# Kernel optimization log

Hardware: AMD Instinct MI355X
Metric: run time of the kernel (lower is better)

Reference implementation:

```python
import jax, jax.numpy as jnp
import numpy as np

B, S, D, H = 2, 2048, 1024, 16
HD = D // H


def setup_inputs() -> dict:
    key = jax.random.key(0)
    ks = jax.random.split(key, 5)
    scale = 0.02
    x = jax.random.normal(ks[0], (B, S, D), dtype=jnp.float32)
    Wq = jax.random.normal(ks[1], (D, D), dtype=jnp.float32) * scale
    Wk = jax.random.normal(ks[2], (D, D), dtype=jnp.float32) * scale
    Wv = jax.random.normal(ks[3], (D, D), dtype=jnp.float32) * scale
    Wo = jax.random.normal(ks[4], (D, D), dtype=jnp.float32) * scale
    z = jnp.zeros((D,), dtype=jnp.float32)
    return {"x": x, "Wq": Wq, "bq": z, "Wk": Wk, "bk": z, "Wv": Wv, "bv": z, "Wo": Wo, "bo": z}


def reference(x, Wq, bq, Wk, bk, Wv, bv, Wo, bo):
    b, s, d = x.shape
    hd = d // H
    # QKV projections -> [b, H, s, hd]
    def heads(W, bias):
        return (x @ W.T + bias).reshape(b, s, H, hd).transpose(0, 2, 1, 3)
    q = heads(Wq, bq)
    k = heads(Wk, bk)
    v = heads(Wv, bv)
    scale = 1.0 / np.sqrt(hd).astype(np.float32)
    attn = scale * jnp.einsum('bhqd,bhkd->bhqk', q, k)  # [b,H,s,s]
    # causal mask (attn dropout p=0 is identity before masking)
    causal = jnp.tril(jnp.ones((s, s), dtype=bool))
    attn = jnp.where(causal[None, None], attn, -jnp.inf)
    attn = jax.nn.softmax(attn, axis=-1)
    ans = jnp.einsum('bhqk,bhkd->bhqd', attn, v)
    ans = ans.transpose(0, 2, 1, 3).reshape(b, s, d)
    return ans @ Wo.T + bo
```

## Files before the change

### kernel.cpp

```cpp
#include <hip/hip_runtime.h>

#define DEV __device__ __forceinline__

typedef __attribute__((ext_vector_type(8))) __bf16 bf16x8;
typedef __attribute__((ext_vector_type(4))) float f32x4;
typedef __attribute__((ext_vector_type(16))) float f32x16;
typedef __attribute__((ext_vector_type(4))) unsigned short u16x4;
typedef __attribute__((ext_vector_type(8))) unsigned short u16x8;
typedef __attribute__((ext_vector_type(2))) unsigned u32x2;

DEV unsigned short f2bf(float f) {
  unsigned u = __builtin_bit_cast(unsigned, f);
  u += 0x7FFFu + ((u >> 16) & 1u);
  return (unsigned short)(u >> 16);
}

DEV f32x4 mfma16(bf16x8 a, bf16x8 b, f32x4 c) {
  return __builtin_amdgcn_mfma_f32_16x16x32_bf16(a, b, c, 0, 0, 0);
}
DEV f32x16 mfma32(bf16x8 a, bf16x8 b, f32x16 c) {
  return __builtin_amdgcn_mfma_f32_32x32x16_bf16(a, b, c, 0, 0, 0);
}

DEV void gload16(const void* g, void* l) {
  __builtin_amdgcn_global_load_lds(
      (const __attribute__((address_space(1))) unsigned int*)g,
      (__attribute__((address_space(3))) unsigned int*)l, 16, 0, 0);
}

DEV void plswap(unsigned& x, unsigned& y) {
#if __has_builtin(__builtin_amdgcn_permlane32_swap)
  u32x2 r = __builtin_amdgcn_permlane32_swap(x, y, false, false);
  x = r[0];
  y = r[1];
#else
  unsigned sx = __shfl_xor(x, 32, 64), sy = __shfl_xor(y, 32, 64);
  int hi = (threadIdx.x & 63) >> 5;
  unsigned nx = hi ? sy : x;
  unsigned ny = hi ? y : sx;
  x = nx;
  y = ny;
#endif
}
DEV float xadd32(float v) {
  unsigned a = __builtin_bit_cast(unsigned, v), b = a;
  plswap(a, b);
  return __builtin_bit_cast(float, a) + __builtin_bit_cast(float, b);
}

__global__ __launch_bounds__(256) void k_cvt_all(
    const float* __restrict__ x,
    const float* __restrict__ Wq, const float* __restrict__ Wk,
    const float* __restrict__ Wv, const float* __restrict__ Wo,
    unsigned short* __restrict__ xb,
    unsigned short* __restrict__ Wqb, unsigned short* __restrict__ Wkb,
    unsigned short* __restrict__ Wvb, unsigned short* __restrict__ Wob) {
  int g = blockIdx.x * 256 + threadIdx.x;
  const float* src;
  unsigned short* dst;
  int loc;
  if (g < 524288) {
    src = x; dst = xb; loc = g;
  } else {
    int r = g - 524288;
    int w = r >> 17;
    loc = r & 131071;
    src = w == 0 ? Wq : w == 1 ? Wk : w == 2 ? Wv : Wo;
    dst = w == 0 ? Wqb : w == 1 ? Wkb : w == 2 ? Wvb : Wob;
  }
  int row = loc >> 7, k8 = loc & 127;
  const f32x4* s = (const f32x4*)(src + ((size_t)row << 10) + (k8 << 3));
  f32x4 a = s[0], b = s[1];
  u16x8 o;
  o[0] = f2bf(a[0]); o[1] = f2bf(a[1]); o[2] = f2bf(a[2]); o[3] = f2bf(a[3]);
  o[4] = f2bf(b[0]); o[5] = f2bf(b[1]); o[6] = f2bf(b[2]); o[7] = f2bf(b[3]);
  *(u16x8*)(dst + ((size_t)row << 10) + ((k8 << 3) ^ ((row & 7) << 3))) = o;
}

DEV void gemm_mainloop(const char* Ag, const char* Bg, char* lds,
                       int lane, int wid, f32x4 acc[4][4]) {
  int g4 = lane >> 4, r16 = lane & 15;
  int wm = wid >> 1, wn = wid & 1;
  int adA[2], adB[2];
#pragma unroll
  for (int ks = 0; ks < 2; ++ks) {
    int swz = ((ks * 4 + g4) ^ (lane & 7)) << 4;
    adA[ks] = (wm * 64 + r16) * 128 + swz;
    adB[ks] = 16384 + (wn * 64 + r16) * 128 + swz;
  }
  int o0 = wid * 4096 + lane * 16;
  int grow[4], ginr[4];
#pragma unroll
  for (int i = 0; i < 4; ++i) {
    grow[i] = (o0 + i * 1024) >> 7;
    ginr[i] = (o0 + i * 1024) & 127;
  }
  auto STAGE = [&](int KT, int BASE) {
#pragma unroll
    for (int i = 0; i < 4; ++i) {
      int oo = o0 + i * 1024;
      size_t gofs = (size_t)grow[i] * 2048 + (size_t)KT * 128 + ginr[i];
      gload16(Ag + gofs, lds + BASE + oo);
      gload16(Bg + gofs, lds + BASE + 16384 + oo);
    }
  };
  STAGE(0, 0);
  __syncthreads();
  for (int kt = 0; kt < 16; ++kt) {
    int cur = (kt & 1) << 15;
    if (kt + 1 < 16) STAGE(kt + 1, cur ^ 32768);
#pragma unroll
    for (int ks = 0; ks < 2; ++ks) {
      bf16x8 af[4], bfr[4];
#pragma unroll
      for (int i = 0; i < 4; ++i) {
        af[i]  = *(const bf16x8*)(lds + cur + adA[ks] + i * 2048);
        bfr[i] = *(const bf16x8*)(lds + cur + adB[ks] + i * 2048);
      }
#pragma unroll
      for (int mi = 0; mi < 4; ++mi)
#pragma unroll
        for (int ni = 0; ni < 4; ++ni)
          acc[mi][ni] = mfma16(af[mi], bfr[ni], acc[mi][ni]);
    }
    __syncthreads();
  }
}

__global__ __launch_bounds__(256) void k_gemm_qkv(
    const unsigned short* __restrict__ xb,
    const unsigned short* __restrict__ Wqb, const unsigned short* __restrict__ Wkb,
    const unsigned short* __restrict__ Wvb,
    const float* __restrict__ bq, const float* __restrict__ bk,
    const float* __restrict__ bv,
    unsigned short* __restrict__ Qb, unsigned short* __restrict__ Kb,
    unsigned short* __restrict__ Vt) {
  __shared__ char lds[65536];
  int tid = threadIdx.x, lane = tid & 63, wid = tid >> 6;
  int bm = blockIdx.x & 31, bn = blockIdx.x >> 5;
  int r0 = bm * 128;
  int colT = bn * 128;
  int which = colT >> 10;
  int ncol = colT & 1023;
  const unsigned short* Wb = which == 0 ? Wqb : which == 1 ? Wkb : Wvb;
  f32x4 acc[4][4] = {};
  gemm_mainloop((const char*)xb + (size_t)r0 * 2048,
                (const char*)Wb + (size_t)ncol * 2048, lds, lane, wid, acc);
  int g4 = lane >> 4, r16 = lane & 15, wm = wid >> 1, wn = wid & 1;
  const float* bias = which == 0 ? bq : which == 1 ? bk : bv;
  float oscale = which == 0 ? 0.18033688f : 1.0f;
  int ncolw = ncol + wn * 64;
#pragma unroll
  for (int ni = 0; ni < 4; ++ni) {
    int gcol = ncolw + ni * 16 + r16;
    float bvv = bias[gcol];
    int h = gcol >> 6, hd = gcol & 63;
#pragma unroll
    for (int mi = 0; mi < 4; ++mi) {
      int growb = r0 + wm * 64 + mi * 16 + g4 * 4;
      int bb = growb >> 11, s0 = growb & 2047;
      if (which == 2) {
        u16x4 pk;
#pragma unroll
        for (int jj = 0; jj < 4; ++jj) pk[jj] = f2bf(acc[mi][ni][jj] + bvv);
        *(u16x4*)(Vt + ((size_t)(bb * 16 + h) * 64 + hd) * 2048 + s0) = pk;
      } else {
        unsigned short* dst = which == 0 ? Qb : Kb;
        size_t base = ((size_t)(bb * 16 + h) * 2048 + s0) * 64 + hd;
#pragma unroll
        for (int jj = 0; jj < 4; ++jj)
          dst[base + (size_t)jj * 64] = f2bf((acc[mi][ni][jj] + bvv) * oscale);
      }
    }
  }
}

__global__ __launch_bounds__(128) void k_attn(
    const unsigned short* __restrict__ Q, const unsigned short* __restrict__ K,
    const unsigned short* __restrict__ Vt, unsigned short* __restrict__ ansb,
    float* __restrict__ PO, float* __restrict__ PL) {
  __shared__ char lds[2 * 8192 + 256];
  int tid = threadIdx.x, lane = tid & 63, wid = tid >> 6;
  int l31 = lane & 31, hi = lane >> 5;
  int bid = blockIdx.x;
  int bh = (bid & 7) * 4 + ((bid >> 3) & 3);
  int sden = bid >> 5;
  int c, j, nseg;
  if (sden < 8)       { c = sden; j = 0; nseg = 1; }
  else if (sden < 24) { int u = sden - 8;  c = 8  + (u >> 1); j = u & 1; nseg = 2; }
  else if (sden < 48) { int u = sden - 24; int q3 = u / 3; c = 16 + q3; j = u - 3 * q3; nseg = 3; }
  else                { int u = sden - 48; c = 24 + (u >> 2); j = u & 3; nseg = 4; }
  int t0 = j * (c + 1) / nseg, t1 = (j + 1) * (c + 1) / nseg;
  bool direct = (nseg == 1);
  int pidx = (bh * 24 + (c - 8)) * 4 + j;
  int b = bh >> 4, h = bh & 15;
  int q0 = c * 64 + wid * 32;
  const unsigned short* Qh = Q + (size_t)bh * (2048 * 64);
  const char* Kg = (const char*)(K + (size_t)bh * (2048 * 64));
  const char* Vg = (const char*)(Vt + (size_t)bh * (64 * 2048));
  char* wb = lds + 16384 + wid * 128;

  int kof[4], ko[4];
#pragma unroll
  for (int i = 0; i < 4; ++i) {
    int o = tid * 16 + i * 2048;
    int row = o >> 7, cc = o & 127;
    kof[i] = o;
    ko[i] = row * 128 + (cc ^ ((row & 7) << 4));
  }

  bf16x8 qf[4];
#pragma unroll
  for (int ks = 0; ks < 4; ++ks)
    qf[ks] = *(const bf16x8*)(Qh + (size_t)(q0 + l31) * 64 + ks * 16 + hi * 8);

  f32x16 O0 = {}, O1 = {}, l16 = {};
  int swzl = (l31 & 7) << 4;
  int hioff = hi * 16;
  const char* Vr0 = Vg + (size_t)l31 * 4096;
  const char* Vr1 = Vg + (size_t)(32 + l31) * 4096;

  auto STAGEK = [&](int T, int BASE) {
    size_t kK = (size_t)T * 8192;
#pragma unroll
    for (int i = 0; i < 4; ++i)
      gload16(Kg + kK + ko[i], lds + BASE + kof[i]);
  };

  STAGEK(t0, 0);
  __syncthreads();
  for (int t = t0; t < t1; ++t) {
    int cur = ((t - t0) & 1) << 13;
    if (t + 1 < t1) STAGEK(t + 1, cur ^ 8192);
    const char* KL = lds + cur;
    const char* Vt0 = Vr0 + (size_t)t * 128;
    const char* Vt1 = Vr1 + (size_t)t * 128;
    f32x16 s0 = {}, s1 = {};
    __builtin_amdgcn_s_setprio(1);
#pragma unroll
    for (int ks = 0; ks < 4; ++ks) {
      bf16x8 kf0 = *(const bf16x8*)(KL + l31 * 128 + ((ks * 32 + hioff) ^ swzl));
      bf16x8 kf1 = *(const bf16x8*)(KL + (32 + l31) * 128 + ((ks * 32 + hioff) ^ swzl));
      s0 = mfma32(kf0, qf[ks], s0);
      s1 = mfma32(kf1, qf[ks], s1);
    }
    __builtin_amdgcn_s_setprio(0);
    if (t == c) {
      int lim2 = q0 + l31 - t * 64 - 4 * hi;
#pragma unroll
      for (int r = 0; r < 16; ++r) {
        int kc = (r & 3) + 8 * (r >> 2);
        if (kc > lim2) s0[r] = -1e30f;
        if (kc + 32 > lim2) s1[r] = -1e30f;
      }
    }
#pragma unroll
    for (int r = 0; r < 16; ++r) {
      s0[r] = __builtin_amdgcn_exp2f(s0[r]);
      s1[r] = __builtin_amdgcn_exp2f(s1[r]);
      l16[r] += s0[r] + s1[r];
    }
    __builtin_amdgcn_s_setprio(1);
#define PV_CHUNK(SV, E, C16) { \
    unsigned x0, x1, y0, y1; \
    asm("v_cvt_pk_bf16_f32 %0, %1, %2" : "=v"(x0) : "v"(SV[8*(E)+0]), "v"(SV[8*(E)+1])); \
    asm("v_cvt_pk_bf16_f32 %0, %1, %2" : "=v"(x1) : "v"(SV[8*(E)+2]), "v"(SV[8*(E)+3])); \
    asm("v_cvt_pk_bf16_f32 %0, %1, %2" : "=v"(y0) : "v"(SV[8*(E)+4]), "v"(SV[8*(E)+5])); \
    asm("v_cvt_pk_bf16_f32 %0, %1, %2" : "=v"(y1) : "v"(SV[8*(E)+6]), "v"(SV[8*(E)+7])); \
    plswap(x0, y0); \
    plswap(x1, y1); \
    union { unsigned u[4]; bf16x8 v; } pf; \
    pf.u[0] = x0; \
    pf.u[1] = x1; \
    pf.u[2] = y0; \
    pf.u[3] = y1; \
    bf16x8 v0 = *(const bf16x8*)(Vt0 + (C16) * 32 + hi * 16); \
    bf16x8 v1 = *(const bf16x8*)(Vt1 + (C16) * 32 + hi * 16); \
    O0 = mfma32(pf.v, v0, O0); \
    O1 = mfma32(pf.v, v1, O1); }
    PV_CHUNK(s0, 0, 0)
    PV_CHUNK(s0, 1, 1)
    PV_CHUNK(s1, 0, 2)
    PV_CHUNK(s1, 1, 3)
#undef PV_CHUNK
    __builtin_amdgcn_s_setprio(0);
    __syncthreads();
  }
  float a[16];
#pragma unroll
  for (int r = 0; r < 16; ++r) a[r] = l16[r];
#pragma unroll
  for (int st2 = 8; st2 >= 1; st2 >>= 1)
#pragma unroll
    for (int i = 0; i < st2; ++i) a[i] += a[i + st2];
  float lf = xadd32(a[0]);
  if (direct) {
    float rl = 1.f / lf;
    if (lane < 32) *(float*)(wb + l31 * 4) = rl;
    asm volatile("s_waitcnt lgkmcnt(0)" ::: "memory");
    f32x4 rv0 = *(const f32x4*)(wb + hioff);
    f32x4 rv1 = *(const f32x4*)(wb + 32 + hioff);
    f32x4 rv2 = *(const f32x4*)(wb + 64 + hioff);
    f32x4 rv3 = *(const f32x4*)(wb + 96 + hioff);
#pragma unroll
    for (int r = 0; r < 16; ++r) {
      float sc = (r < 4 ? rv0 : r < 8 ? rv1 : r < 12 ? rv2 : rv3)[r & 3];
      int rowl = q0 + (r & 3) + 8 * (r >> 2) + 4 * hi;
      int rowg = (b << 11) + rowl;
      int cswz = (rowl & 7) << 3;
      int cg0 = (h << 6) + l31;
      int cg1 = (h << 6) + 32 + l31;
      ansb[(size_t)rowg * 1024 + (cg0 ^ cswz)] = f2bf(O0[r] * sc);
      ansb[(size_t)rowg * 1024 + (cg1 ^ cswz)] = f2bf(O1[r] * sc);
    }
  } else {
    float* po = PO + (size_t)pidx * 4096;
#pragma unroll
    for (int r = 0; r < 16; ++r) {
      int rowl = wid * 32 + (r & 3) + 8 * (r >> 2) + 4 * hi;
      po[rowl * 64 + l31] = O0[r];
      po[rowl * 64 + 32 + l31] = O1[r];
    }
    if (hi == 0) PL[pidx * 64 + wid * 32 + l31] = lf;
  }
}

__global__ __launch_bounds__(256) void k_attn_combine(
    const float* __restrict__ PO, const float* __restrict__ PL,
    unsigned short* __restrict__ ansb) {
  int bid = blockIdx.x;
  int bh = bid & 31, cc = 8 + (bid >> 5);
  int nseg = cc < 16 ? 2 : cc < 24 ? 3 : 4;
  int b = bh >> 4, h = bh & 15;
  int t = threadIdx.x;
  int r = t >> 2, c4 = (t & 3) << 4;
  int pbase = (bh * 24 + (cc - 8)) * 4;
  f32x4 s0 = {}, s1 = {}, s2 = {}, s3 = {};
  float lsum = 0.f;
  for (int j = 0; j < nseg; ++j) {
    const float* A = PO + (size_t)(pbase + j) * 4096 + r * 64 + c4;
    s0 += *(const f32x4*)(A + 0);
    s1 += *(const f32x4*)(A + 4);
    s2 += *(const f32x4*)(A + 8);
    s3 += *(const f32x4*)(A + 12);
    lsum += PL[(pbase + j) * 64 + r];
  }
  float rl = 1.f / lsum;
  u16x8 o0, o1;
#pragma unroll
  for (int j = 0; j < 4; ++j) {
    o0[j] = f2bf(s0[j] * rl);
    o0[4 + j] = f2bf(s1[j] * rl);
    o1[j] = f2bf(s2[j] * rl);
    o1[4 + j] = f2bf(s3[j] * rl);
  }
  int rowg = (b << 11) + cc * 64 + r;
  int colg = (h << 6) + c4;
  int cswz = (rowg & 7) << 3;
  *(u16x8*)(ansb + (size_t)rowg * 1024 + (colg ^ cswz)) = o0;
  *(u16x8*)(ansb + (size_t)rowg * 1024 + ((colg + 8) ^ cswz)) = o1;
}

__global__ __launch_bounds__(256) void k_gemm_out(
    const unsigned short* __restrict__ ansb, const unsigned short* __restrict__ Wob,
    const float* __restrict__ bo, float* __restrict__ out) {
  __shared__ char lds[65536];
  int tid = threadIdx.x, lane = tid & 63, wid = tid >> 6;
  int bm = blockIdx.x & 31, bn = blockIdx.x >> 5;
  int r0 = bm * 128, c0 = bn * 128;
  f32x4 acc[4][4] = {};
  gemm_mainloop((const char*)ansb + (size_t)r0 * 2048,
                (const char*)Wob + (size_t)c0 * 2048, lds, lane, wid, acc);
  int g4 = lane >> 4, r16 = lane & 15, wm = wid >> 1, wn = wid & 1;
#pragma unroll
  for (int ni = 0; ni < 4; ++ni) {
    int gcol = c0 + wn * 64 + ni * 16 + r16;
    float bvv = bo[gcol];
#pragma unroll
    for (int mi = 0; mi < 4; ++mi) {
      int growb = r0 + wm * 64 + mi * 16 + g4 * 4;
#pragma unroll
      for (int jj = 0; jj < 4; ++jj)
        out[(size_t)(growb + jj) * 1024 + gcol] = acc[mi][ni][jj] + bvv;
    }
  }
}

extern "C" void kernel_launch(void* const* d_in, const int* in_sizes, int n_in,
                              void* d_out, int out_size, void* d_ws, size_t ws_size,
                              hipStream_t stream) {
  const float* x  = (const float*)d_in[0];
  const float* Wq = (const float*)d_in[1];
  const float* bq = (const float*)d_in[2];
  const float* Wk = (const float*)d_in[3];
  const float* bk = (const float*)d_in[4];
  const float* Wv = (const float*)d_in[5];
  const float* bv = (const float*)d_in[6];
  const float* Wo = (const float*)d_in[7];
  const float* bo = (const float*)d_in[8];
  char* ws = (char*)d_ws;
  unsigned short* xb   = (unsigned short*)(ws);
  unsigned short* ansb = (unsigned short*)(ws);
  unsigned short* Wqb  = (unsigned short*)(ws + (8u  << 20));
  unsigned short* Wkb  = (unsigned short*)(ws + (10u << 20));
  unsigned short* Wvb  = (unsigned short*)(ws + (12u << 20));
  unsigned short* Wob  = (unsigned short*)(ws + (14u << 20));
  unsigned short* Qb   = (unsigned short*)(ws + (16u << 20));
  unsigned short* Kb   = (unsigned short*)(ws + (24u << 20));
  unsigned short* Vt   = (unsigned short*)(ws + (32u << 20));
  float*          PO   = (float*)(ws + (40u << 20));
  float*          PL   = (float*)(ws + (88u << 20));

  k_cvt_all<<<4096, 256, 0, stream>>>(x, Wq, Wk, Wv, Wo, xb, Wqb, Wkb, Wvb, Wob);
  k_gemm_qkv<<<768, 256, 0, stream>>>(xb, Wqb, Wkb, Wvb, bq, bk, bv, Qb, Kb, Vt);
  k_attn<<<2560, 128, 0, stream>>>(Qb, Kb, Vt, ansb, PO, PL);
  k_attn_combine<<<768, 256, 0, stream>>>(PO, PL, ansb);
  k_gemm_out<<<256, 256, 0, stream>>>(ansb, Wob, bo, (float*)d_out);
}
```

Baseline: 125.2 us.

## Stage V tiles through LDS and use table-driven causal work partition

The attention kernel now loads both K and V tiles into swizzled LDS each iteration, instead of double-buffering K and reading V fragments straight from global memory. It waits on all loads and a barrier before compute, so the K prefetch overlap is gone. The block-to-segment mapping is replaced by a constant lookup table that splits the causal query chunks unevenly across blocks to balance work. The gain relies on coalesced V staging and better load balance outweighing the lost overlap.

```diff
diff --git a/kernel.cpp b/kernel.cpp
--- a/kernel.cpp
+++ b/kernel.cpp
@@ -179,19 +179,45 @@
     const unsigned short* __restrict__ Q, const unsigned short* __restrict__ K,
     const unsigned short* __restrict__ Vt, unsigned short* __restrict__ ansb,
     float* __restrict__ PO, float* __restrict__ PL) {
-  __shared__ char lds[2 * 8192 + 256];
+  __shared__ char lds[16384 + 256];
+#define SG(c, a, bb2, jj) \
+  ((unsigned)(c) | ((unsigned)(a) << 8) | ((unsigned)(bb2) << 16) | ((unsigned)(jj) << 24))
+  static const unsigned SEGT[80] = {
+    SG(31,0,8,0),  SG(31,8,16,1), SG(31,16,24,2), SG(31,24,32,3),
+    SG(30,7,15,1), SG(30,15,23,2), SG(30,23,31,3),
+    SG(29,7,15,1), SG(29,22,30,3), SG(28,21,29,3),
+    SG(23,0,8,0),  SG(23,8,16,1), SG(23,16,24,2),
+    SG(22,7,15,1), SG(22,15,23,2), SG(21,14,22,2),
+    SG(15,0,8,0),  SG(15,8,16,1), SG(14,7,15,1),  SG(7,0,8,0),
+    SG(30,0,7,0),  SG(29,0,7,0),  SG(29,15,22,2),
+    SG(28,0,7,0),  SG(28,7,14,1), SG(28,14,21,2),
+    SG(27,0,7,0),  SG(27,7,14,1), SG(27,14,21,2), SG(27,21,28,3),
+    SG(26,6,13,1), SG(26,13,20,2), SG(26,20,27,3),
+    SG(25,6,13,1), SG(25,19,26,3), SG(24,18,25,3),
+    SG(22,0,7,0),  SG(21,0,7,0),  SG(21,7,14,1),
+    SG(20,0,7,0),  SG(20,7,14,1), SG(20,14,21,2),
+    SG(19,6,13,1), SG(19,13,20,2), SG(18,12,19,2),
+    SG(14,0,7,0),  SG(13,0,7,0),  SG(13,7,14,1),
+    SG(12,6,13,1), SG(6,0,7,0),
+    SG(26,0,6,0),  SG(25,0,6,0),  SG(25,13,19,2),
+    SG(24,0,6,0),  SG(24,6,12,1), SG(24,12,18,2),
+    SG(19,0,6,0),  SG(18,0,6,0),  SG(18,6,12,1),
+    SG(17,0,6,0),  SG(17,6,12,1), SG(17,12,18,2),
+    SG(16,5,11,1), SG(16,11,17,2),
+    SG(12,0,6,0),  SG(11,0,6,0),  SG(11,6,12,1),
+    SG(10,5,11,1), SG(5,0,6,0),
+    SG(16,0,5,0), SG(10,0,5,0), SG(9,0,5,0), SG(9,5,10,1), SG(8,4,9,1),
+    SG(4,0,5,0),
+    SG(8,0,4,0), SG(3,0,4,0), SG(2,0,3,0), SG(1,0,2,0), SG(0,0,1,0)
+  };
+#undef SG
   int tid = threadIdx.x, lane = tid & 63, wid = tid >> 6;
   int l31 = lane & 31, hi = lane >> 5;
   int bid = blockIdx.x;
   int bh = (bid & 7) * 4 + ((bid >> 3) & 3);
-  int sden = bid >> 5;
-  int c, j, nseg;
-  if (sden < 8)       { c = sden; j = 0; nseg = 1; }
-  else if (sden < 24) { int u = sden - 8;  c = 8  + (u >> 1); j = u & 1; nseg = 2; }
-  else if (sden < 48) { int u = sden - 24; int q3 = u / 3; c = 16 + q3; j = u - 3 * q3; nseg = 3; }
-  else                { int u = sden - 48; c = 24 + (u >> 2); j = u & 3; nseg = 4; }
-  int t0 = j * (c + 1) / nseg, t1 = (j + 1) * (c + 1) / nseg;
-  bool direct = (nseg == 1);
+  unsigned se = SEGT[bid >> 5];
+  int c = se & 255, t0 = (se >> 8) & 255, t1 = (se >> 16) & 255, j = se >> 24;
+  bool direct = (c < 8);
   int pidx = (bh * 24 + (c - 8)) * 4 + j;
   int b = bh >> 4, h = bh & 15;
   int q0 = c * 64 + wid * 32;
@@ -200,13 +226,15 @@
   const char* Vg = (const char*)(Vt + (size_t)bh * (64 * 2048));
   char* wb = lds + 16384 + wid * 128;
 
-  int kof[4], ko[4];
+  int kof[4], ko[4], vo[4];
 #pragma unroll
   for (int i = 0; i < 4; ++i) {
     int o = tid * 16 + i * 2048;
     int row = o >> 7, cc = o & 127;
+    int sc = cc ^ ((row & 7) << 4);
     kof[i] = o;
-    ko[i] = row * 128 + (cc ^ ((row & 7) << 4));
+    ko[i] = row * 128 + sc;
+    vo[i] = row * 4096 + sc;
   }
 
   bf16x8 qf[4];
@@ -217,24 +245,20 @@
   f32x16 O0 = {}, O1 = {}, l16 = {};
   int swzl = (l31 & 7) << 4;
   int hioff = hi * 16;
-  const char* Vr0 = Vg + (size_t)l31 * 4096;
-  const char* Vr1 = Vg + (size_t)(32 + l31) * 4096;
-
-  auto STAGEK = [&](int T, int BASE) {
-    size_t kK = (size_t)T * 8192;
-#pragma unroll
-    for (int i = 0; i < 4; ++i)
-      gload16(Kg + kK + ko[i], lds + BASE + kof[i]);
-  };
-
-  STAGEK(t0, 0);
-  __syncthreads();
+
   for (int t = t0; t < t1; ++t) {
-    int cur = ((t - t0) & 1) << 13;
-    if (t + 1 < t1) STAGEK(t + 1, cur ^ 8192);
-    const char* KL = lds + cur;
-    const char* Vt0 = Vr0 + (size_t)t * 128;
-    const char* Vt1 = Vr1 + (size_t)t * 128;
+    size_t kK = (size_t)t * 8192;
+    size_t kV = (size_t)t * 128;
+#pragma unroll
+    for (int i = 0; i < 4; ++i) {
+      gload16(Kg + kK + ko[i], lds + kof[i]);
+      gload16(Vg + kV + vo[i], lds + 8192 + kof[i]);
+    }
+    asm volatile("s_waitcnt vmcnt(0)" ::: "memory");
+    __builtin_amdgcn_s_barrier();
+    __builtin_amdgcn_sched_barrier(0);
+    const char* KL = lds;
+    const char* VL = lds + 8192;
     f32x16 s0 = {}, s1 = {};
     __builtin_amdgcn_s_setprio(1);
 #pragma unroll
@@ -274,8 +298,8 @@
     pf.u[1] = x1; \
     pf.u[2] = y0; \
     pf.u[3] = y1; \
-    bf16x8 v0 = *(const bf16x8*)(Vt0 + (C16) * 32 + hi * 16); \
-    bf16x8 v1 = *(const bf16x8*)(Vt1 + (C16) * 32 + hi * 16); \
+    bf16x8 v0 = *(const bf16x8*)(VL + l31 * 128 + (((C16) * 32 + hioff) ^ swzl)); \
+    bf16x8 v1 = *(const bf16x8*)(VL + (32 + l31) * 128 + (((C16) * 32 + hioff) ^ swzl)); \
     O0 = mfma32(pf.v, v0, O0); \
     O1 = mfma32(pf.v, v1, O1); }
     PV_CHUNK(s0, 0, 0)
```

New measurement: 109.9 us. -12.2%, faster.

## Restructure attention into single-wave 32-row tiles with LDS-staged V and finer barriers

Applied to the files above, without the earlier changes.

The attention kernel now runs one wave per block on 32-query tiles with 32-key steps. It stages both K and V tiles into swizzled LDS via async loads instead of reading V directly from global memory, and drops the block-wide barrier. The split-K schedule is rebuilt for the new tile count, heaviest tiles first, and the combine kernel is adapted to match. The GEMM mainloop replaces __syncthreads with explicit vmcnt/lgkmcnt waits, raw barriers and setprio around the MFMAs, to overlap the next stage's loads better. The cost is a doubled grid and more partial outputs, and per-block MFMA work is smaller, which may reduce efficiency.

```diff
diff --git a/kernel.cpp b/kernel.cpp
--- a/kernel.cpp
+++ b/kernel.cpp
@@ -105,10 +105,16 @@
     }
   };
   STAGE(0, 0);
-  __syncthreads();
   for (int kt = 0; kt < 16; ++kt) {
     int cur = (kt & 1) << 15;
-    if (kt + 1 < 16) STAGE(kt + 1, cur ^ 32768);
+    if (kt + 1 < 16) {
+      STAGE(kt + 1, cur ^ 32768);
+      asm volatile("s_waitcnt vmcnt(8)" ::: "memory");
+    } else {
+      asm volatile("s_waitcnt vmcnt(0)" ::: "memory");
+    }
+    __builtin_amdgcn_s_barrier();
+    __builtin_amdgcn_sched_barrier(0);
 #pragma unroll
     for (int ks = 0; ks < 2; ++ks) {
       bf16x8 af[4], bfr[4];
@@ -117,13 +123,17 @@
         af[i]  = *(const bf16x8*)(lds + cur + adA[ks] + i * 2048);
         bfr[i] = *(const bf16x8*)(lds + cur + adB[ks] + i * 2048);
       }
+      __builtin_amdgcn_s_setprio(1);
 #pragma unroll
       for (int mi = 0; mi < 4; ++mi)
 #pragma unroll
         for (int ni = 0; ni < 4; ++ni)
           acc[mi][ni] = mfma16(af[mi], bfr[ni], acc[mi][ni]);
-    }
-    __syncthreads();
+      __builtin_amdgcn_s_setprio(0);
+    }
+    asm volatile("s_waitcnt lgkmcnt(0)" ::: "memory");
+    __builtin_amdgcn_sched_barrier(0);
+    __builtin_amdgcn_s_barrier();
   }
 }
 
@@ -175,38 +185,40 @@
   }
 }
 
-__global__ __launch_bounds__(128) void k_attn(
+__global__ __launch_bounds__(64) void k_attn(
     const unsigned short* __restrict__ Q, const unsigned short* __restrict__ K,
     const unsigned short* __restrict__ Vt, unsigned short* __restrict__ ansb,
     float* __restrict__ PO, float* __restrict__ PL) {
-  __shared__ char lds[2 * 8192 + 256];
-  int tid = threadIdx.x, lane = tid & 63, wid = tid >> 6;
+  __shared__ char lds[2 * 8192 + 128];
+  int lane = threadIdx.x & 63;
   int l31 = lane & 31, hi = lane >> 5;
   int bid = blockIdx.x;
   int bh = (bid & 7) * 4 + ((bid >> 3) & 3);
   int sden = bid >> 5;
-  int c, j, nseg;
-  if (sden < 8)       { c = sden; j = 0; nseg = 1; }
-  else if (sden < 24) { int u = sden - 8;  c = 8  + (u >> 1); j = u & 1; nseg = 2; }
-  else if (sden < 48) { int u = sden - 24; int q3 = u / 3; c = 16 + q3; j = u - 3 * q3; nseg = 3; }
-  else                { int u = sden - 48; c = 24 + (u >> 2); j = u & 3; nseg = 4; }
-  int t0 = j * (c + 1) / nseg, t1 = (j + 1) * (c + 1) / nseg;
+  int cp, j, nseg;
+  if (sden < 8)        { cp = 15 - sden;          j = 0;              nseg = 1; }
+  else if (sden < 72)  { int u = sden - 8;   cp = 63 - (u >> 2); j = u & 3;        nseg = 4; }
+  else if (sden < 120) { int u = sden - 72;  int q3 = u / 3; cp = 47 - q3; j = u - 3 * q3; nseg = 3; }
+  else if (sden < 152) { int u = sden - 120; cp = 31 - (u >> 1); j = u & 1;        nseg = 2; }
+  else                 { int u = sden - 152; cp = 7 - u;           j = 0;          nseg = 1; }
+  int t0 = j * (cp + 1) / nseg, t1 = (j + 1) * (cp + 1) / nseg;
   bool direct = (nseg == 1);
-  int pidx = (bh * 24 + (c - 8)) * 4 + j;
+  int pidx = (bh * 48 + (cp - 16)) * 4 + j;
   int b = bh >> 4, h = bh & 15;
-  int q0 = c * 64 + wid * 32;
+  int q0 = cp * 32;
   const unsigned short* Qh = Q + (size_t)bh * (2048 * 64);
   const char* Kg = (const char*)(K + (size_t)bh * (2048 * 64));
   const char* Vg = (const char*)(Vt + (size_t)bh * (64 * 2048));
-  char* wb = lds + 16384 + wid * 128;
-
-  int kof[4], ko[4];
+
+  int kof[4], ko[4], vo[4];
 #pragma unroll
   for (int i = 0; i < 4; ++i) {
-    int o = tid * 16 + i * 2048;
+    int o = lane * 16 + i * 1024;
     int row = o >> 7, cc = o & 127;
     kof[i] = o;
     ko[i] = row * 128 + (cc ^ ((row & 7) << 4));
+    int vr = o >> 6, vc = o & 63;
+    vo[i] = vr * 4096 + (vc ^ (((vr >> 1) & 3) << 4));
   }
 
   bf16x8 qf[4];
@@ -216,49 +228,52 @@
 
   f32x16 O0 = {}, O1 = {}, l16 = {};
   int swzl = (l31 & 7) << 4;
+  int vswz = ((l31 >> 1) & 3) << 4;
   int hioff = hi * 16;
-  const char* Vr0 = Vg + (size_t)l31 * 4096;
-  const char* Vr1 = Vg + (size_t)(32 + l31) * 4096;
-
-  auto STAGEK = [&](int T, int BASE) {
-    size_t kK = (size_t)T * 8192;
-#pragma unroll
-    for (int i = 0; i < 4; ++i)
+
+  auto STAGEA = [&](int T, int BASE) {
+    size_t kK = (size_t)T * 4096;
+    size_t kV = (size_t)T * 64;
+#pragma unroll
+    for (int i = 0; i < 4; ++i) {
       gload16(Kg + kK + ko[i], lds + BASE + kof[i]);
+      gload16(Vg + kV + vo[i], lds + BASE + 4096 + kof[i]);
+    }
   };
 
-  STAGEK(t0, 0);
-  __syncthreads();
+  STAGEA(t0, 0);
   for (int t = t0; t < t1; ++t) {
     int cur = ((t - t0) & 1) << 13;
-    if (t + 1 < t1) STAGEK(t + 1, cur ^ 8192);
+    if (t + 1 < t1) {
+      asm volatile("s_waitcnt lgkmcnt(0)" ::: "memory");
+      STAGEA(t + 1, cur ^ 8192);
+      asm volatile("s_waitcnt vmcnt(8)" ::: "memory");
+    } else {
+      asm volatile("s_waitcnt vmcnt(0)" ::: "memory");
+    }
+    __builtin_amdgcn_sched_barrier(0);
     const char* KL = lds + cur;
-    const char* Vt0 = Vr0 + (size_t)t * 128;
-    const char* Vt1 = Vr1 + (size_t)t * 128;
-    f32x16 s0 = {}, s1 = {};
+    const char* VL = KL + 4096;
+    f32x16 s0 = {};
     __builtin_amdgcn_s_setprio(1);
 #pragma unroll
     for (int ks = 0; ks < 4; ++ks) {
       bf16x8 kf0 = *(const bf16x8*)(KL + l31 * 128 + ((ks * 32 + hioff) ^ swzl));
-      bf16x8 kf1 = *(const bf16x8*)(KL + (32 + l31) * 128 + ((ks * 32 + hioff) ^ swzl));
       s0 = mfma32(kf0, qf[ks], s0);
-      s1 = mfma32(kf1, qf[ks], s1);
     }
     __builtin_amdgcn_s_setprio(0);
-    if (t == c) {
-      int lim2 = q0 + l31 - t * 64 - 4 * hi;
+    if (t == cp) {
+      int lim2 = l31 - 4 * hi;
 #pragma unroll
       for (int r = 0; r < 16; ++r) {
         int kc = (r & 3) + 8 * (r >> 2);
         if (kc > lim2) s0[r] = -1e30f;
-        if (kc + 32 > lim2) s1[r] = -1e30f;
       }
     }
 #pragma unroll
     for (int r = 0; r < 16; ++r) {
       s0[r] = __builtin_amdgcn_exp2f(s0[r]);
-      s1[r] = __builtin_amdgcn_exp2f(s1[r]);
-      l16[r] += s0[r] + s1[r];
+      l16[r] += s0[r];
     }
     __builtin_amdgcn_s_setprio(1);
 #define PV_CHUNK(SV, E, C16) { \
@@ -274,17 +289,14 @@
     pf.u[1] = x1; \
     pf.u[2] = y0; \
     pf.u[3] = y1; \
-    bf16x8 v0 = *(const bf16x8*)(Vt0 + (C16) * 32 + hi * 16); \
-    bf16x8 v1 = *(const bf16x8*)(Vt1 + (C16) * 32 + hi * 16); \
+    bf16x8 v0 = *(const bf16x8*)(VL + l31 * 64 + (((C16) * 32 + hioff) ^ vswz)); \
+    bf16x8 v1 = *(const bf16x8*)(VL + (32 + l31) * 64 + (((C16) * 32 + hioff) ^ vswz)); \
     O0 = mfma32(pf.v, v0, O0); \
     O1 = mfma32(pf.v, v1, O1); }
     PV_CHUNK(s0, 0, 0)
     PV_CHUNK(s0, 1, 1)
-    PV_CHUNK(s1, 0, 2)
-    PV_CHUNK(s1, 1, 3)
 #undef PV_CHUNK
     __builtin_amdgcn_s_setprio(0);
-    __syncthreads();
   }
   float a[16];
 #pragma unroll
@@ -295,6 +307,8 @@
     for (int i = 0; i < st2; ++i) a[i] += a[i + st2];
   float lf = xadd32(a[0]);
   if (direct) {
+    asm volatile("s_waitcnt lgkmcnt(0)" ::: "memory");
+    char* wb = lds;
     float rl = 1.f / lf;
     if (lane < 32) *(float*)(wb + l31 * 4) = rl;
     asm volatile("s_waitcnt lgkmcnt(0)" ::: "memory");
@@ -314,36 +328,36 @@
       ansb[(size_t)rowg * 1024 + (cg1 ^ cswz)] = f2bf(O1[r] * sc);
     }
   } else {
-    float* po = PO + (size_t)pidx * 4096;
+    float* po = PO + (size_t)pidx * 2048;
 #pragma unroll
     for (int r = 0; r < 16; ++r) {
-      int rowl = wid * 32 + (r & 3) + 8 * (r >> 2) + 4 * hi;
+      int rowl = (r & 3) + 8 * (r >> 2) + 4 * hi;
       po[rowl * 64 + l31] = O0[r];
       po[rowl * 64 + 32 + l31] = O1[r];
     }
-    if (hi == 0) PL[pidx * 64 + wid * 32 + l31] = lf;
-  }
-}
-
-__global__ __launch_bounds__(256) void k_attn_combine(
+    if (hi == 0) PL[pidx * 32 + l31] = lf;
+  }
+}
+
+__global__ __launch_bounds__(128) void k_attn_combine(
     const float* __restrict__ PO, const float* __restrict__ PL,
     unsigned short* __restrict__ ansb) {
   int bid = blockIdx.x;
-  int bh = bid & 31, cc = 8 + (bid >> 5);
-  int nseg = cc < 16 ? 2 : cc < 24 ? 3 : 4;
+  int bh = bid & 31, cp = 16 + (bid >> 5);
+  int nseg = cp < 32 ? 2 : cp < 48 ? 3 : 4;
   int b = bh >> 4, h = bh & 15;
   int t = threadIdx.x;
   int r = t >> 2, c4 = (t & 3) << 4;
-  int pbase = (bh * 24 + (cc - 8)) * 4;
+  int pbase = (bh * 48 + (cp - 16)) * 4;
   f32x4 s0 = {}, s1 = {}, s2 = {}, s3 = {};
   float lsum = 0.f;
   for (int j = 0; j < nseg; ++j) {
-    const float* A = PO + (size_t)(pbase + j) * 4096 + r * 64 + c4;
+    const float* A = PO + (size_t)(pbase + j) * 2048 + r * 64 + c4;
     s0 += *(const f32x4*)(A + 0);
     s1 += *(const f32x4*)(A + 4);
     s2 += *(const f32x4*)(A + 8);
     s3 += *(const f32x4*)(A + 12);
-    lsum += PL[(pbase + j) * 64 + r];
+    lsum += PL[(pbase + j) * 32 + r];
   }
   float rl = 1.f / lsum;
   u16x8 o0, o1;
@@ -354,7 +368,7 @@
     o1[j] = f2bf(s2[j] * rl);
     o1[4 + j] = f2bf(s3[j] * rl);
   }
-  int rowg = (b << 11) + cc * 64 + r;
+  int rowg = (b << 11) + cp * 32 + r;
   int colg = (h << 6) + c4;
   int cswz = (rowg & 7) << 3;
   *(u16x8*)(ansb + (size_t)rowg * 1024 + (colg ^ cswz)) = o0;
@@ -413,7 +427,7 @@
 
   k_cvt_all<<<4096, 256, 0, stream>>>(x, Wq, Wk, Wv, Wo, xb, Wqb, Wkb, Wvb, Wob);
   k_gemm_qkv<<<768, 256, 0, stream>>>(xb, Wqb, Wkb, Wvb, bq, bk, bv, Qb, Kb, Vt);
-  k_attn<<<2560, 128, 0, stream>>>(Qb, Kb, Vt, ansb, PO, PL);
-  k_attn_combine<<<768, 256, 0, stream>>>(PO, PL, ansb);
+  k_attn<<<5120, 64, 0, stream>>>(Qb, Kb, Vt, ansb, PO, PL);
+  k_attn_combine<<<1536, 128, 0, stream>>>(PO, PL, ansb);
   k_gemm_out<<<256, 256, 0, stream>>>(ansb, Wob, bo, (float*)d_out);
 }
```

New measurement: 109.6 us. 1.14x faster.
